# Performance work log

Measured on AMD Instinct MI355X. Metric: run time of the kernel, lower is better.

The kernel has to match this reference:

```python
import jax, jax.numpy as jnp
import numpy as np

# ---- config (YOLOv4-style, TRAIN_SIZE=608, P2..P5) ----
STRIDES = (4.0, 8.0, 16.0, 32.0)
ANCHORS = np.array([
    [[12, 16], [19, 36], [40, 28], [36, 75]],
    [[36, 75], [76, 55], [72, 146], [142, 110]],
    [[72, 146], [142, 110], [192, 243], [459, 401]],
    [[142, 110], [192, 243], [300, 300], [459, 401]],
], dtype=np.float32)  # [LEVELS, NUM_ANCHORS, 2]
MAX_PROP = 100
SCORE_THRESH = 0.25
IOU_THRESH = 0.5


def decode_prediction(p, anchors, stride):
    # p: [b, A, h, w, 6] -> [b, A*h*w, 5] with xyxy + score
    b, A, h, w, _ = p.shape
    txy, twh, conf, cls = p[..., :2], p[..., 2:4], p[..., 4:5], p[..., 5:6]
    gx, gy = jnp.meshgrid(jnp.arange(w, dtype=p.dtype), jnp.arange(h, dtype=p.dtype))
    grid = jnp.stack([gx, gy], axis=-1)[None, None]  # [1,1,h,w,2]
    xy = (jax.nn.sigmoid(txy) + grid) * stride
    wh = jnp.exp(twh) * anchors[None, :, None, None, :]
    score = jax.nn.sigmoid(conf) * jax.nn.sigmoid(cls)
    x1y1 = xy - 0.5 * wh
    x2y2 = xy + 0.5 * wh
    out = jnp.concatenate([x1y1, x2y2, score], axis=-1)  # [b,A,h,w,5]
    return out.reshape(b, A * h * w, 5)


def _iou_one_vs_all(box, boxes):
    # box: [4], boxes: [N,4] (xyxy)
    lt = jnp.maximum(box[:2], boxes[:, :2])
    rb = jnp.minimum(box[2:], boxes[:, 2:])
    wh = jnp.maximum(rb - lt, 0.0)
    inter = wh[:, 0] * wh[:, 1]
    a1 = jnp.maximum(box[2] - box[0], 0.0) * jnp.maximum(box[3] - box[1], 0.0)
    a2 = jnp.maximum(boxes[:, 2] - boxes[:, 0], 0.0) * jnp.maximum(boxes[:, 3] - boxes[:, 1], 0.0)
    return inter / (a1 + a2 - inter + 1e-9)


def _nms_single(boxes, scores):
    # greedy NMS, padded to MAX_PROP with zero rows
    s0 = jnp.where(scores >= SCORE_THRESH, scores, 0.0)

    def step(s, _):
        i = jnp.argmax(s)
        sc = s[i]
        box = boxes[i]
        keep = sc > 0.0
        row = jnp.where(keep, jnp.concatenate([box, sc[None]]), jnp.zeros(5, boxes.dtype))
        iou = _iou_one_vs_all(box, boxes)
        s = jnp.where((iou > IOU_THRESH) & keep, 0.0, s)
        s = s.at[i].set(0.0)
        return s, row

    _, props = jax.lax.scan(step, s0, None, length=MAX_PROP)
    return props  # [MAX_PROP, 5]


def entry_stop_gradients(t, mask):
    # gradient flows only through entries where mask==1
    return jax.lax.stop_gradient(t) * (1.0 - mask) + t * mask


def _forward(p2, p3, p4, p5):
    anchors = jnp.asarray(ANCHORS)
    d2 = decode_prediction(p2, anchors[0], STRIDES[0])
    d3 = decode_prediction(p3, anchors[1], STRIDES[1])
    d4 = decode_prediction(p4, anchors[2], STRIDES[2])
    d5 = decode_prediction(p5, anchors[3], STRIDES[3])
    proposals = jnp.concatenate([d2, d3, d4, d5], axis=1)  # [b, N, 5]
    proposals = jax.vmap(lambda pr: _nms_single(pr[:, :4], pr[:, 4]))(proposals)  # [b, MAX_PROP, 5]
    mask = (jnp.sum(proposals[..., :4], axis=-1) != 0.0).astype(proposals.dtype)[..., None]
    return entry_stop_gradients(proposals, mask)


def setup_inputs() -> dict:
    key = jax.random.key(0)
    k2, k3, k4, k5 = jax.random.split(key, 4)
    b, A, ch = 32, 4, 6
    return {
        "p2": jax.random.normal(k2, (b, A, 152, 152, ch), dtype=jnp.float32),
        "p3": jax.random.normal(k3, (b, A, 76, 76, ch), dtype=jnp.float32),
        "p4": jax.random.normal(k4, (b, A, 38, 38, ch), dtype=jnp.float32),
        "p5": jax.random.normal(k5, (b, A, 19, 19, ch), dtype=jnp.float32),
    }


def reference(p2, p3, p4, p5):
    return _forward(p2, p3, p4, p5)
```

## Files before the change

### kernel.cpp

```cpp
#include <hip/hip_runtime.h>
#include <cstdint>
#include <cstddef>

typedef unsigned int u32;
typedef unsigned long long u64;

#define NTOT 122740
#define NQ   30685
#define NPAIR 61370
#define KTOP 1024
#define WIN  256
#define NBIN 512
#define SCORE_T 0.25f
#define TBITS 0x3E800000u
#define WS_SCORES 65536


__device__ __forceinline__ float sigm(float x) { return 1.0f / (1.0f + expf(-x)); }

__device__ __forceinline__ int score_bin(u32 bits) {
  return min(NBIN - 1, 1 + (int)((bits - TBITS) >> 15));
}

__device__ float4 decode_box_from_gidx(u32 gidx, int b,
    const float* __restrict__ p2, const float* __restrict__ p3,
    const float* __restrict__ p4, const float* __restrict__ p5)
{
  const float* p; int t, H, W; float stride;
  float aw0, ah0, aw1, ah1, aw2, ah2, aw3, ah3;
  if (gidx < 92416u) {
    p = p2 + (size_t)b * 92416 * 6; t = (int)gidx; H = 152; W = 152; stride = 4.0f;
    aw0=12.f; ah0=16.f; aw1=19.f; ah1=36.f; aw2=40.f; ah2=28.f; aw3=36.f; ah3=75.f;
  } else if (gidx < 115520u) {
    p = p3 + (size_t)b * 23104 * 6; t = (int)(gidx - 92416u); H = 76; W = 76; stride = 8.0f;
    aw0=36.f; ah0=75.f; aw1=76.f; ah1=55.f; aw2=72.f; ah2=146.f; aw3=142.f; ah3=110.f;
  } else if (gidx < 121296u) {
    p = p4 + (size_t)b * 5776 * 6; t = (int)(gidx - 115520u); H = 38; W = 38; stride = 16.0f;
    aw0=72.f; ah0=146.f; aw1=142.f; ah1=110.f; aw2=192.f; ah2=243.f; aw3=459.f; ah3=401.f;
  } else {
    p = p5 + (size_t)b * 1444 * 6; t = (int)(gidx - 121296u); H = 19; W = 19; stride = 32.0f;
    aw0=142.f; ah0=110.f; aw1=192.f; ah1=243.f; aw2=300.f; ah2=300.f; aw3=459.f; ah3=401.f;
  }
  int HW = H * W;
  int a = t / HW;
  int r = t - a * HW;
  int y = r / W;
  int x = r - y * W;
  const float* q = p + (size_t)t * 6;
  float2 t01 = *(const float2*)(q + 0);
  float2 t23 = *(const float2*)(q + 2);
  float cx = (sigm(t01.x) + (float)x) * stride;
  float cy = (sigm(t01.y) + (float)y) * stride;
  float aw = (a == 0) ? aw0 : (a == 1) ? aw1 : (a == 2) ? aw2 : aw3;
  float ah = (a == 0) ? ah0 : (a == 1) ? ah1 : (a == 2) ? ah2 : ah3;
  float bw = expf(t23.x) * aw;
  float bh = expf(t23.y) * ah;
  return make_float4(cx - 0.5f * bw, cy - 0.5f * bh, cx + 0.5f * bw, cy + 0.5f * bh);
}

__device__ __forceinline__ bool iou_gt(float4 A, float4 B) {
  float ltx = fmaxf(A.x, B.x), lty = fmaxf(A.y, B.y);
  float rbx = fminf(A.z, B.z), rby = fminf(A.w, B.w);
  float w = fmaxf(rbx - ltx, 0.0f), h = fmaxf(rby - lty, 0.0f);
  float inter = w * h;
  float a1 = fmaxf(A.z - A.x, 0.0f) * fmaxf(A.w - A.y, 0.0f);
  float a2 = fmaxf(B.z - B.x, 0.0f) * fmaxf(B.w - B.y, 0.0f);
  float iou = inter / (a1 + a2 - inter + 1e-9f);
  return iou > 0.5f;
}

__device__ __forceinline__ u64 shflx_u64(u64 v, int m) {
  u32 lo = (u32)v, hi = (u32)(v >> 32);
  lo = (u32)__shfl_xor((int)lo, m, 64);
  hi = (u32)__shfl_xor((int)hi, m, 64);
  return ((u64)hi << 32) | lo;
}
__device__ __forceinline__ u64 ce_pick(u64 v, u64 p, int i, int jj, int kk) {
  bool up = ((i & kk) == 0);
  bool low = ((i & jj) == 0);
  u64 mn = (v < p) ? v : p;
  u64 mx = (v < p) ? p : v;
  return (low == up) ? mn : mx;
}
__device__ __forceinline__ u64 ce_shfl(u64 v, int i, int jj, int kk) {
  u64 p = shflx_u64(v, jj);
  return ce_pick(v, p, i, jj, kk);
}

__global__ __launch_bounds__(256)
void decode_score_hist(const float* __restrict__ p2, const float* __restrict__ p3,
                       const float* __restrict__ p4, const float* __restrict__ p5,
                       u32* __restrict__ scores, u32* __restrict__ hist)
{
  __shared__ u32 lhist[NBIN];
  const int tid = threadIdx.x;
  const int b = blockIdx.y;
  for (int i = tid; i < NBIN; i += 256) lhist[i] = 0u;
  __syncthreads();

  uint2* srow = (uint2*)(scores + (size_t)b * NTOT);
  const int pbase = blockIdx.x * 2048;
  #pragma unroll 4
  for (int k = 0; k < 8; ++k) {
    int P = pbase + k * 256 + tid;
    if (P < NPAIR) {
      int t0 = 2 * P;
      const float* p; int l0, LN;
      if (t0 < 92416)       { p = p2; l0 = t0;          LN = 92416; }
      else if (t0 < 115520) { p = p3; l0 = t0 - 92416;  LN = 23104; }
      else if (t0 < 121296) { p = p4; l0 = t0 - 115520; LN = 5776;  }
      else                  { p = p5; l0 = t0 - 121296; LN = 1444;  }
      const float* q = p + ((size_t)b * LN + (size_t)l0) * 6 + 4;
      float4 v1 = *(const float4*)(q);
      float4 v2 = *(const float4*)(q + 4);
      float s0 = sigm(v1.x) * sigm(v1.y);
      float s1 = sigm(v2.z) * sigm(v2.w);
      u32 b0 = (s0 >= SCORE_T) ? __float_as_uint(s0) : 0u;
      u32 b1 = (s1 >= SCORE_T) ? __float_as_uint(s1) : 0u;
      srow[P] = make_uint2(b0, b1);
      if (b0) atomicAdd(&lhist[score_bin(b0)], 1u);
      if (b1) atomicAdd(&lhist[score_bin(b1)], 1u);
    }
  }
  __syncthreads();
  u32* gh = hist + (size_t)b * NBIN;
  for (int i = tid; i < NBIN; i += 256) {
    u32 v = lhist[i];
    if (v) atomicAdd(&gh[i], v);
  }
}

__global__ __launch_bounds__(1024, 1)
void sort_nms_kernel(const u32* __restrict__ scores, const u32* __restrict__ hist,
                     const float* __restrict__ p2, const float* __restrict__ p3,
                     const float* __restrict__ p4, const float* __restrict__ p5,
                     float* __restrict__ out)
{
  const int b = blockIdx.x;
  const int tid = threadIdx.x;
  const int lane = tid & 63;

  __shared__ u32 shist[NBIN];
  __shared__ u32 sc[NBIN];
  __shared__ uint2 cand[KTOP];
  __shared__ u64 skey[KTOP];
  __shared__ float4 sbox[WIN];
  __shared__ u64 smat[WIN * 4];
  __shared__ float4 selbox[100];
  __shared__ u32 sellist[100];
  __shared__ u32 s_cnt;
  __shared__ int s_B, s_nsel, s_slow;

  const u32* gh = hist + (size_t)b * NBIN;
  if (tid < NBIN) { u32 h = gh[tid]; shist[tid] = h; sc[tid] = h; }
  if (tid == 0) { s_cnt = 0u; s_B = NBIN - 1; s_slow = 0; }
  __syncthreads();
  for (int off = 1; off < NBIN; off <<= 1) {
    u32 v = 0;
    if (tid < NBIN && tid + off < NBIN) v = sc[tid + off];
    __syncthreads();
    if (tid < NBIN) sc[tid] += v;
    __syncthreads();
  }
  if (tid < NBIN) {
    if (sc[tid] <= (u32)KTOP && (tid == 0 || sc[tid - 1] > (u32)KTOP))
      s_B = max((int)tid, 1);
  }
  __syncthreads();
  const int B = s_B;

  const uint4* sp = (const uint4*)(scores + (size_t)b * NTOT);
  for (int i = tid; i < NQ; i += 1024) {
    uint4 v = sp[i];
    u32 c4[4] = { v.x, v.y, v.z, v.w };
    #pragma unroll
    for (int c = 0; c < 4; ++c) {
      u32 bits = c4[c];
      bool pred = bits && (score_bin(bits) >= B);
      u64 m = __ballot(pred);
      if (m) {
        int leader = (int)__ffsll((unsigned long long)m) - 1;
        u32 base = 0;
        if (lane == leader) base = atomicAdd(&s_cnt, (u32)__popcll(m));
        base = (u32)__shfl((int)base, leader, 64);
        if (pred) {
          u32 pos = base + (u32)__popcll(m & ((1ull << lane) - 1ull));
          if (pos < (u32)KTOP) cand[pos] = make_uint2(bits, (u32)(4 * i + c));
        }
      }
    }
  }
  __syncthreads();
  const int n = min((int)s_cnt, KTOP);

  u64 v;
  if (tid < n) { uint2 pr = cand[tid]; v = ~(((u64)pr.x << 32) | (u32)(~pr.y)); }
  else v = ~0ull;
  const int i = tid;
  #pragma unroll
  for (int kk = 2; kk <= 64; kk <<= 1)
    #pragma unroll
    for (int jj = kk >> 1; jj > 0; jj >>= 1)
      v = ce_shfl(v, i, jj, kk);
  for (int kk = 128; kk <= KTOP; kk <<= 1) {
    for (int jj = kk >> 1; jj >= 64; jj >>= 1) {
      skey[i] = v; __syncthreads();
      u64 p = skey[i ^ jj]; __syncthreads();
      v = ce_pick(v, p, i, jj, kk);
    }
    #pragma unroll
    for (int jj = 32; jj > 0; jj >>= 1) v = ce_shfl(v, i, jj, kk);
  }
  skey[i] = v;
  __syncthreads();

  const int Wn = min(n, WIN);

  if (tid < WIN) {
    sbox[tid] = (tid < Wn) ? decode_box_from_gidx(~(u32)(~skey[tid]), b, p2, p3, p4, p5)
                           : make_float4(0.f, 0.f, 0.f, 0.f);
  }
  __syncthreads();

  {
    int row = tid >> 2, word = tid & 3;
    u64 bits = 0;
    if (row < Wn) {
      float4 A = sbox[row];
      int j0 = word * 64, je = min(64, Wn - j0);
      for (int j = 0; j < je; ++j)
        if (iou_gt(A, sbox[j0 + j])) bits |= (1ull << j);
    }
    smat[tid] = bits;
  }
  __syncthreads();

  if (tid < 64) {
    u64 m0[4], m1[4], m2[4], m3[4];
    #pragma unroll
    for (int d = 0; d < 4; ++d) {
      m0[d] = smat[(lane      ) * 4 + d];
      m1[d] = smat[(lane +  64) * 4 + d];
      m2[d] = smat[(lane + 128) * 4 + d];
      m3[d] = smat[(lane + 192) * 4 + d];
    }
    bool f0 = lane < Wn, f1 = lane + 64 < Wn, f2 = lane + 128 < Wn, f3 = lane + 192 < Wn;
    int sel = 0;
    while (sel < 100) {
      u64 b0 = __ballot(f0), b1 = __ballot(f1), b2 = __ballot(f2), b3 = __ballot(f3);
      int p;
      if (b0)      p = (int)__ffsll((unsigned long long)b0) - 1;
      else if (b1) p = 64 + (int)__ffsll((unsigned long long)b1) - 1;
      else if (b2) p = 128 + (int)__ffsll((unsigned long long)b2) - 1;
      else if (b3) p = 192 + (int)__ffsll((unsigned long long)b3) - 1;
      else break;
      if (lane == 0) sellist[sel] = (u32)p;
      sel++;
      int d = p >> 6, sh = p & 63;
      u64 r0 = (d == 0) ? m0[0] : (d == 1) ? m0[1] : (d == 2) ? m0[2] : m0[3];
      u64 r1 = (d == 0) ? m1[0] : (d == 1) ? m1[1] : (d == 2) ? m1[2] : m1[3];
      u64 r2 = (d == 0) ? m2[0] : (d == 1) ? m2[1] : (d == 2) ? m2[2] : m2[3];
      u64 r3 = (d == 0) ? m3[0] : (d == 1) ? m3[1] : (d == 2) ? m3[2] : m3[3];
      f0 = f0 && !((r0 >> sh) & 1);
      f1 = f1 && !((r1 >> sh) & 1);
      f2 = f2 && !((r2 >> sh) & 1);
      f3 = f3 && !((r3 >> sh) & 1);
    }
    if (lane == 0) { s_nsel = sel; s_slow = (sel < 100 && n > WIN) ? 1 : 0; }
  }
  __syncthreads();

  const int nsel0 = s_nsel;
  if (tid < nsel0) {
    u32 p = sellist[tid];
    float4 bx = sbox[p];
    u64 kcomp = ~skey[p];
    float scs = __uint_as_float((u32)(kcomp >> 32));
    float* orow = out + (size_t)b * 500 + (size_t)tid * 5;
    orow[0] = bx.x; orow[1] = bx.y; orow[2] = bx.z; orow[3] = bx.w; orow[4] = scs;
  }

  if (s_slow) {
    if (tid < nsel0) selbox[tid] = sbox[sellist[tid]];
    __syncthreads();
    if (tid < 64) {
      int sel = nsel0;
      for (int p = WIN; p < n && sel < 100; ++p) {
        u64 kcomp = ~skey[p];
        float4 box = decode_box_from_gidx(~(u32)kcomp, b, p2, p3, p4, p5);
        bool hit = false;
        if (lane < sel) hit = iou_gt(selbox[lane], box);
        if (lane + 64 < sel) hit = hit || iou_gt(selbox[lane + 64], box);
        u64 anyhit = __ballot(hit);
        if (anyhit == 0ull) {
          if (lane == 0) {
            selbox[sel] = box;
            float scs = __uint_as_float((u32)(kcomp >> 32));
            float* orow = out + (size_t)b * 500 + (size_t)sel * 5;
            orow[0] = box.x; orow[1] = box.y; orow[2] = box.z; orow[3] = box.w; orow[4] = scs;
          }
          sel++;
        }
      }
      if (lane == 0) s_nsel = sel;
    }
  }
  __syncthreads();

  const int nsel = s_nsel;
  for (int k = tid; k < (100 - nsel) * 5; k += 1024)
    out[(size_t)b * 500 + (size_t)nsel * 5 + k] = 0.0f;
}

extern "C" void kernel_launch(void* const* d_in, const int* in_sizes, int n_in,
                              void* d_out, int out_size, void* d_ws, size_t ws_size,
                              hipStream_t stream) {
  const float* p2 = (const float*)d_in[0];
  const float* p3 = (const float*)d_in[1];
  const float* p4 = (const float*)d_in[2];
  const float* p5 = (const float*)d_in[3];
  float* out = (float*)d_out;

  u32* hist   = (u32*)d_ws;
  u32* scores = (u32*)((unsigned char*)d_ws + WS_SCORES);

  hipMemsetAsync(hist, 0, WS_SCORES, stream);
  decode_score_hist<<<dim3(30, 32), 256, 0, stream>>>(p2, p3, p4, p5, scores, hist);
  sort_nms_kernel<<<32, 1024, 0, stream>>>(scores, hist, p2, p3, p4, p5, out);
}
```

Baseline: 196.8 us.

## Split candidate filtering into multi-block kernel and stage decode loads through LDS

Moves the histogram-threshold scan and candidate compaction out of the single-block-per-image sort/NMS kernel into a new filter kernel with 15 blocks per image that writes to a global compact buffer using atomic counters. The decode kernel now loads the full 6-float records as coalesced float4s into shared memory before computing scores. The aim is to parallelise the 120K-element scan that previously ran on only 32 blocks, and to improve load coalescing. This adds a kernel launch, and candidate order in the compact buffer becomes nondeterministic, although the subsequent sort restores a deterministic order. The threshold-bin computation is also changed to work over pairs of bins.

```diff
diff --git a/kernel.cpp b/kernel.cpp
--- a/kernel.cpp
+++ b/kernel.cpp
@@ -13,7 +13,11 @@
 #define NBIN 512
 #define SCORE_T 0.25f
 #define TBITS 0x3E800000u
-#define WS_SCORES 65536
+#define CSTRIDE 64
+
+#define WS_COUNTERS 65536
+#define WS_COMPACT  73728
+#define WS_SCORES   335872
 
 
 __device__ __forceinline__ float sigm(float x) { return 1.0f / (1.0f + expf(-x)); }
@@ -92,37 +96,48 @@
                        const float* __restrict__ p4, const float* __restrict__ p5,
                        u32* __restrict__ scores, u32* __restrict__ hist)
 {
+  __shared__ float4 lstage[768];
   __shared__ u32 lhist[NBIN];
   const int tid = threadIdx.x;
   const int b = blockIdx.y;
   for (int i = tid; i < NBIN; i += 256) lhist[i] = 0u;
-  __syncthreads();
 
   uint2* srow = (uint2*)(scores + (size_t)b * NTOT);
-  const int pbase = blockIdx.x * 2048;
-  #pragma unroll 4
-  for (int k = 0; k < 8; ++k) {
-    int P = pbase + k * 256 + tid;
-    if (P < NPAIR) {
-      int t0 = 2 * P;
-      const float* p; int l0, LN;
-      if (t0 < 92416)       { p = p2; l0 = t0;          LN = 92416; }
-      else if (t0 < 115520) { p = p3; l0 = t0 - 92416;  LN = 23104; }
-      else if (t0 < 121296) { p = p4; l0 = t0 - 115520; LN = 5776;  }
-      else                  { p = p5; l0 = t0 - 121296; LN = 1444;  }
-      const float* q = p + ((size_t)b * LN + (size_t)l0) * 6 + 4;
-      float4 v1 = *(const float4*)(q);
-      float4 v2 = *(const float4*)(q + 4);
-      float s0 = sigm(v1.x) * sigm(v1.y);
-      float s1 = sigm(v2.z) * sigm(v2.w);
+  const float* lsf = (const float*)lstage;
+
+  for (int c = 0; c < 8; ++c) {
+    const int pb = blockIdx.x * 2048 + c * 256;
+    #pragma unroll
+    for (int j = 0; j < 3; ++j) {
+      int F = j * 256 + tid;
+      int Pl = F / 3;
+      int comp = F - 3 * Pl;
+      int P = pb + Pl;
+      if (P < NPAIR) {
+        int t0 = 2 * P;
+        const float* p; int l0, LN;
+        if (t0 < 92416)       { p = p2; l0 = t0;          LN = 92416; }
+        else if (t0 < 115520) { p = p3; l0 = t0 - 92416;  LN = 23104; }
+        else if (t0 < 121296) { p = p4; l0 = t0 - 115520; LN = 5776;  }
+        else                  { p = p5; l0 = t0 - 121296; LN = 1444;  }
+        lstage[F] = *(const float4*)(p + ((size_t)b * LN + (size_t)l0) * 6 + comp * 4);
+      }
+    }
+    __syncthreads();
+    int pr = pb + tid;
+    if (pr < NPAIR) {
+      float2 cc0 = *(const float2*)(lsf + 12 * tid + 4);
+      float2 cc1 = *(const float2*)(lsf + 12 * tid + 10);
+      float s0 = sigm(cc0.x) * sigm(cc0.y);
+      float s1 = sigm(cc1.x) * sigm(cc1.y);
       u32 b0 = (s0 >= SCORE_T) ? __float_as_uint(s0) : 0u;
       u32 b1 = (s1 >= SCORE_T) ? __float_as_uint(s1) : 0u;
-      srow[P] = make_uint2(b0, b1);
+      srow[pr] = make_uint2(b0, b1);
       if (b0) atomicAdd(&lhist[score_bin(b0)], 1u);
       if (b1) atomicAdd(&lhist[score_bin(b1)], 1u);
     }
-  }
-  __syncthreads();
+    __syncthreads();
+  }
   u32* gh = hist + (size_t)b * NBIN;
   for (int i = tid; i < NBIN; i += 256) {
     u32 v = lhist[i];
@@ -130,8 +145,73 @@
   }
 }
 
+__global__ __launch_bounds__(256)
+void filter_kernel(const u32* __restrict__ scores, const u32* __restrict__ hist,
+                   u32* __restrict__ counters, uint2* __restrict__ compact)
+{
+  __shared__ u32 shist[NBIN];
+  __shared__ u32 scan[256];
+  __shared__ uint2 cand[KTOP];
+  __shared__ u32 s_cnt, s_base;
+  __shared__ int s_B;
+  const int tid = threadIdx.x;
+  const int b = blockIdx.y;
+
+  const u32* gh = hist + (size_t)b * NBIN;
+  shist[tid] = gh[tid];
+  shist[tid + 256] = gh[tid + 256];
+  if (tid == 0) { s_cnt = 0u; s_B = NBIN - 1; }
+  __syncthreads();
+
+  scan[tid] = shist[2 * tid] + shist[2 * tid + 1];
+  __syncthreads();
+  for (int off = 1; off < 256; off <<= 1) {
+    u32 v = (tid + off < 256) ? scan[tid + off] : 0u;
+    __syncthreads();
+    scan[tid] += v;
+    __syncthreads();
+  }
+  if (tid == 0 && scan[0] <= (u32)KTOP) s_B = 1;
+  {
+    u32 nxt = (tid < 255) ? scan[tid + 1] : 0u;
+    if (scan[tid] > (u32)KTOP && nxt <= (u32)KTOP) {
+      int Bv = 2 * tid + 2;
+      if (nxt + shist[2 * tid + 1] <= (u32)KTOP) Bv = 2 * tid + 1;
+      s_B = Bv;
+    }
+  }
+  __syncthreads();
+  const int B = max(s_B, 1);
+
+  const uint4* sp = (const uint4*)(scores + (size_t)b * NTOT);
+  const int i0 = blockIdx.x * 2048;
+  const int i1 = min(i0 + 2048, NQ);
+  for (int i = i0 + tid; i < i1; i += 256) {
+    uint4 v = sp[i];
+    u32 c4[4] = { v.x, v.y, v.z, v.w };
+    #pragma unroll
+    for (int c = 0; c < 4; ++c) {
+      u32 bits = c4[c];
+      if (bits && score_bin(bits) >= B) {
+        u32 pos = atomicAdd(&s_cnt, 1u);
+        if (pos < (u32)KTOP) cand[pos] = make_uint2(bits, (u32)(4 * i + c));
+      }
+    }
+  }
+  __syncthreads();
+  const u32 m = min(s_cnt, (u32)KTOP);
+  if (tid == 0) s_base = m ? atomicAdd(&counters[(size_t)b * CSTRIDE], m) : 0u;
+  __syncthreads();
+  const u32 gbase = s_base;
+  uint2* crow = compact + (size_t)b * KTOP;
+  for (u32 i = tid; i < m; i += 256) {
+    u32 dst = gbase + i;
+    if (dst < (u32)KTOP) crow[dst] = cand[i];
+  }
+}
+
 __global__ __launch_bounds__(1024, 1)
-void sort_nms_kernel(const u32* __restrict__ scores, const u32* __restrict__ hist,
+void sort_nms_kernel(const uint2* __restrict__ compact, const u32* __restrict__ counters,
                      const float* __restrict__ p2, const float* __restrict__ p3,
                      const float* __restrict__ p4, const float* __restrict__ p5,
                      float* __restrict__ out)
@@ -140,62 +220,21 @@
   const int tid = threadIdx.x;
   const int lane = tid & 63;
 
-  __shared__ u32 shist[NBIN];
-  __shared__ u32 sc[NBIN];
-  __shared__ uint2 cand[KTOP];
   __shared__ u64 skey[KTOP];
   __shared__ float4 sbox[WIN];
   __shared__ u64 smat[WIN * 4];
   __shared__ float4 selbox[100];
   __shared__ u32 sellist[100];
-  __shared__ u32 s_cnt;
-  __shared__ int s_B, s_nsel, s_slow;
-
-  const u32* gh = hist + (size_t)b * NBIN;
-  if (tid < NBIN) { u32 h = gh[tid]; shist[tid] = h; sc[tid] = h; }
-  if (tid == 0) { s_cnt = 0u; s_B = NBIN - 1; s_slow = 0; }
-  __syncthreads();
-  for (int off = 1; off < NBIN; off <<= 1) {
-    u32 v = 0;
-    if (tid < NBIN && tid + off < NBIN) v = sc[tid + off];
-    __syncthreads();
-    if (tid < NBIN) sc[tid] += v;
-    __syncthreads();
-  }
-  if (tid < NBIN) {
-    if (sc[tid] <= (u32)KTOP && (tid == 0 || sc[tid - 1] > (u32)KTOP))
-      s_B = max((int)tid, 1);
-  }
-  __syncthreads();
-  const int B = s_B;
-
-  const uint4* sp = (const uint4*)(scores + (size_t)b * NTOT);
-  for (int i = tid; i < NQ; i += 1024) {
-    uint4 v = sp[i];
-    u32 c4[4] = { v.x, v.y, v.z, v.w };
-    #pragma unroll
-    for (int c = 0; c < 4; ++c) {
-      u32 bits = c4[c];
-      bool pred = bits && (score_bin(bits) >= B);
-      u64 m = __ballot(pred);
-      if (m) {
-        int leader = (int)__ffsll((unsigned long long)m) - 1;
-        u32 base = 0;
-        if (lane == leader) base = atomicAdd(&s_cnt, (u32)__popcll(m));
-        base = (u32)__shfl((int)base, leader, 64);
-        if (pred) {
-          u32 pos = base + (u32)__popcll(m & ((1ull << lane) - 1ull));
-          if (pos < (u32)KTOP) cand[pos] = make_uint2(bits, (u32)(4 * i + c));
-        }
-      }
-    }
-  }
-  __syncthreads();
-  const int n = min((int)s_cnt, KTOP);
+  __shared__ int s_nsel, s_slow;
+
+  const int n = min((int)counters[(size_t)b * CSTRIDE], KTOP);
+  const uint2* crow = compact + (size_t)b * KTOP;
+  if (tid == 0) s_slow = 0;
 
   u64 v;
-  if (tid < n) { uint2 pr = cand[tid]; v = ~(((u64)pr.x << 32) | (u32)(~pr.y)); }
+  if (tid < n) { uint2 pr = crow[tid]; v = ~(((u64)pr.x << 32) | (u32)(~pr.y)); }
   else v = ~0ull;
+
   const int i = tid;
   #pragma unroll
   for (int kk = 2; kk <= 64; kk <<= 1)
@@ -274,8 +313,7 @@
   if (tid < nsel0) {
     u32 p = sellist[tid];
     float4 bx = sbox[p];
-    u64 kcomp = ~skey[p];
-    float scs = __uint_as_float((u32)(kcomp >> 32));
+    float scs = __uint_as_float((u32)((~skey[p]) >> 32));
     float* orow = out + (size_t)b * 500 + (size_t)tid * 5;
     orow[0] = bx.x; orow[1] = bx.y; orow[2] = bx.z; orow[3] = bx.w; orow[4] = scs;
   }
@@ -321,10 +359,14 @@
   const float* p5 = (const float*)d_in[3];
   float* out = (float*)d_out;
 
-  u32* hist   = (u32*)d_ws;
-  u32* scores = (u32*)((unsigned char*)d_ws + WS_SCORES);
-
-  hipMemsetAsync(hist, 0, WS_SCORES, stream);
+  unsigned char* w = (unsigned char*)d_ws;
+  u32*   hist     = (u32*)w;
+  u32*   counters = (u32*)(w + WS_COUNTERS);
+  uint2* compact  = (uint2*)(w + WS_COMPACT);
+  u32*   scores   = (u32*)(w + WS_SCORES);
+
+  hipMemsetAsync(w, 0, WS_COMPACT, stream);
   decode_score_hist<<<dim3(30, 32), 256, 0, stream>>>(p2, p3, p4, p5, scores, hist);
-  sort_nms_kernel<<<32, 1024, 0, stream>>>(scores, hist, p2, p3, p4, p5, out);
-}
+  filter_kernel<<<dim3(15, 32), 256, 0, stream>>>(scores, hist, counters, compact);
+  sort_nms_kernel<<<32, 1024, 0, stream>>>(compact, counters, p2, p3, p4, p5, out);
+}
```

New measurement: 185.4 us. 5.8% less time.
